# Kernel optimization log

Hardware: AMD Instinct MI355X
Metric: run time of the kernel (lower is better)

## Reference

```python
import jax, jax.numpy as jnp
import numpy as np

T, B, E, H = 2048, 2, 1024, 16
DH = E // H
SCALE = DH ** -0.5
NEG = jnp.finfo(jnp.float32).min


def setup_inputs() -> dict:
    key = jax.random.key(0)
    ks = jax.random.split(key, 10)
    s = 0.02
    query = jax.random.normal(ks[0], (T, B, E), dtype=jnp.float32)
    key_padding_mask = jax.random.randint(ks[1], (B, T), 0, 2).astype(bool)
    # causal additive mask, broadcastable over (bsz, heads, tgt, src)
    causal = jnp.triu(jnp.ones((T, T), dtype=bool), k=1)
    attn_mask = jnp.where(causal, NEG, 0.0).astype(jnp.float32)[None, None]
    Wq = jax.random.normal(ks[2], (E, E), jnp.float32) * s
    bq = jax.random.normal(ks[3], (E,), jnp.float32) * s
    Wk = jax.random.normal(ks[4], (E, E), jnp.float32) * s
    bk = jax.random.normal(ks[5], (E,), jnp.float32) * s
    Wv = jax.random.normal(ks[6], (E, E), jnp.float32) * s
    bv = jax.random.normal(ks[7], (E,), jnp.float32) * s
    Wo = jax.random.normal(ks[8], (E, E), jnp.float32) * s
    bo = jax.random.normal(ks[9], (E,), jnp.float32) * s
    return {"query": query, "key_padding_mask": key_padding_mask, "attn_mask": attn_mask,
            "Wq": Wq, "bq": bq, "Wk": Wk, "bk": bk, "Wv": Wv, "bv": bv, "Wo": Wo, "bo": bo}


def _heads(x):
    # [T, B, E] -> [B, H, T, DH]
    return x.reshape(T, B, H, DH).transpose(1, 2, 0, 3)


def reference(query, key_padding_mask, attn_mask, Wq, bq, Wk, bk, Wv, bv, Wo, bo):
    # projections (torch Linear: x @ W.T + b); q scaled as in module
    q = _heads((query @ Wq.T + bq) * SCALE)          # [B,H,T,DH]
    k = _heads(query @ Wk.T + bk)                    # [B,H,S,DH] (self-attn: S=T)
    v = _heads(query @ Wv.T + bv)
    scores = jnp.einsum('bhtd,bhsd->bhts', q, k)     # [B,H,T,S]
    scores = scores + attn_mask                      # additive causal mask
    # key_padding_mask True -> masked_fill with dtype min
    scores = jnp.where(key_padding_mask[:, None, None, :], NEG, scores)
    probs = jax.nn.softmax(scores, axis=-1)
    ctx = jnp.einsum('bhts,bhsd->bhtd', probs, v)    # [B,H,T,DH]
    ctx = ctx.transpose(2, 0, 1, 3).reshape(T, B, E) # back to [T,B,E]
    return ctx @ Wo.T + bo
```

## Files before the change

kernel.cpp:

```cpp
#include <hip/hip_runtime.h>
#include <hip/hip_bf16.h>
#include <stdint.h>

typedef unsigned short u16;
typedef uint32_t u32;
typedef unsigned long long u64;
typedef __attribute__((ext_vector_type(8))) short bf16x8;
typedef __attribute__((ext_vector_type(4))) float f32x4;
typedef __attribute__((ext_vector_type(16))) float f32x16;
typedef __attribute__((ext_vector_type(2))) unsigned int u32x2;
typedef __attribute__((ext_vector_type(4))) u32 u32x4;

#define T_SEQ 2048

__device__ __forceinline__ float bf2f(u16 u) {
  union { u32 i; float f; } v; v.i = ((u32)u) << 16; return v.f;
}
__device__ __forceinline__ u16 f2bf(float f) {
  union { float f; u32 i; } v; v.f = f;
  u32 u = v.i;
  return (u16)((u + 0x7fffu + ((u >> 16) & 1u)) >> 16);
}

#if __has_builtin(__builtin_amdgcn_exp2f)
#define EXP2F(x) __builtin_amdgcn_exp2f(x)
#else
#define EXP2F(x) exp2f(x)
#endif

__device__ __forceinline__ u32 permpack(float lo, float hi) {
#if __has_builtin(__builtin_amdgcn_perm)
  return __builtin_amdgcn_perm(__float_as_uint(hi), __float_as_uint(lo), 0x07060302u);
#else
  return (__float_as_uint(hi) & 0xFFFF0000u) | (__float_as_uint(lo) >> 16);
#endif
}

__device__ __forceinline__ void plswap(u32& a, u32& b) {
#if __has_builtin(__builtin_amdgcn_permlane32_swap)
  u32x2 r = __builtin_amdgcn_permlane32_swap(a, b, false, false);
  a = r[0]; b = r[1];
#else
  u32 ra = __shfl_xor(a, 32, 64), rb = __shfl_xor(b, 32, 64);
  const bool hi_ = (threadIdx.x & 32) != 0;
  u32 na = hi_ ? rb : a;
  u32 nb = hi_ ? b : ra;
  a = na; b = nb;
#endif
}
__device__ __forceinline__ float othhalf(float x, bool ishi) {
  u32 a = __float_as_uint(x), b = a;
  plswap(a, b);
  return __uint_as_float(ishi ? a : b);
}

__device__ __forceinline__ void gload_lds16(const void* g, void* l) {
  __builtin_amdgcn_global_load_lds(
      (const __attribute__((address_space(1))) void*)g,
      (__attribute__((address_space(3))) void*)l, 16, 0, 0);
}

__global__ __launch_bounds__(256) void cvt_kernel(const float* __restrict__ src,
                                                  u16* __restrict__ dst, int n) {
  int i = (blockIdx.x * 256 + threadIdx.x) * 4;
  if (i + 3 < n) {
    const float4 v = *(const float4*)(src + i);
    ushort4 o;
    o.x = f2bf(v.x); o.y = f2bf(v.y); o.z = f2bf(v.z); o.w = f2bf(v.w);
    *(ushort4*)(dst + i) = o;
  }
}

__global__ __launch_bounds__(256) void cvt4_kernel(
    const float* __restrict__ s0, const float* __restrict__ s1,
    const float* __restrict__ s2, const float* __restrict__ s3,
    u16* __restrict__ dst) {
  const int z = blockIdx.y;
  const float* src = (z == 0) ? s0 : (z == 1) ? s1 : (z == 2) ? s2 : s3;
  int i = (blockIdx.x * 256 + threadIdx.x) * 4;
  const float4 v = *(const float4*)(src + i);
  ushort4 o;
  o.x = f2bf(v.x); o.y = f2bf(v.y); o.z = f2bf(v.z); o.w = f2bf(v.w);
  *(ushort4*)(dst + (size_t)z * 1048576 + i) = o;
}

__device__ __forceinline__ void gemm_core_128x128(
    f32x4 acc[2][4], const u16* __restrict__ A, const u16* __restrict__ Bw,
    int bm, int bn, u16* As, u16* Bs)
{
  const int tid = threadIdx.x;
  const int w = tid >> 6, lane = tid & 63, g = lane >> 4, c = lane & 15;
  const int wr = (w & 3) * 32, wc = (w >> 2) * 64;

  auto stage = [&](int buf, int k0) {
    #pragma unroll
    for (int is = 0; is < 2; ++is) {
      int o = (is*8 + w)*1024 + lane*16;
      int row = o >> 7, c16 = (o >> 4) & 7;
      gload_lds16(A + (size_t)(bm*128 + row)*1024 + k0 + (c16 ^ (row & 7))*8,
                  (char*)As + buf*16384 + (is*8 + w)*1024);
    }
    #pragma unroll
    for (int is = 0; is < 2; ++is) {
      int o = (is*8 + w)*1024 + lane*16;
      int row = o >> 7, c16 = (o >> 4) & 7;
      gload_lds16(Bw + (size_t)(bn*128 + row)*1024 + k0 + (c16 ^ (row & 7))*8,
                  (char*)Bs + buf*16384 + (is*8 + w)*1024);
    }
  };

  stage(0, 0);
  asm volatile("s_waitcnt vmcnt(0)" ::: "memory");
  __syncthreads();

  for (int k0 = 0; k0 < 1024; k0 += 64) {
    const int cur = (k0 >> 6) & 1, nxt = cur ^ 1;
    const bool more = (k0 + 64 < 1024);
    if (more) stage(nxt, k0 + 64);

    bf16x8 af[2][2], bfr[4][2];
    #pragma unroll
    for (int mf = 0; mf < 2; ++mf)
      #pragma unroll
      for (int kc = 0; kc < 2; ++kc) {
        int row = wr + mf*16 + c;
        int colb = kc*64 + g*16;
        af[mf][kc] = *(const bf16x8*)((const char*)As + cur*16384 + row*128 + (colb ^ ((row & 7) << 4)));
      }
    #pragma unroll
    for (int nf = 0; nf < 4; ++nf)
      #pragma unroll
      for (int kc = 0; kc < 2; ++kc) {
        int row = wc + nf*16 + c;
        int colb = kc*64 + g*16;
        bfr[nf][kc] = *(const bf16x8*)((const char*)Bs + cur*16384 + row*128 + (colb ^ ((row & 7) << 4)));
      }
    #pragma unroll
    for (int mf = 0; mf < 2; ++mf)
      #pragma unroll
      for (int nf = 0; nf < 4; ++nf)
        #pragma unroll
        for (int kc = 0; kc < 2; ++kc)
          acc[mf][nf] = __builtin_amdgcn_mfma_f32_16x16x32_bf16(
              af[mf][kc], bfr[nf][kc], acc[mf][nf], 0, 0, 0);

    if (more) {
      asm volatile("s_waitcnt vmcnt(0)" ::: "memory");
      __syncthreads();
    }
  }
}

__global__ __launch_bounds__(512, 2) void gemm_qkv(
    const u16* __restrict__ Abf, const u16* __restrict__ Wbf,
    const float* __restrict__ bq, const float* __restrict__ bk,
    const float* __restrict__ bv, u16* __restrict__ qkvh)
{
  __shared__ __align__(16) u16 As[2][128*64];
  __shared__ __align__(16) u16 Bs[2][128*64];
  f32x4 acc[2][4];
  #pragma unroll
  for (int mf = 0; mf < 2; ++mf)
    #pragma unroll
    for (int nf = 0; nf < 4; ++nf) acc[mf][nf] = (f32x4){0.f,0.f,0.f,0.f};
  const int bx = blockIdx.x;
  const int bm = (bx & 7) * 4 + (bx >> 3);
  gemm_core_128x128(acc, Abf, Wbf, bm, blockIdx.y, &As[0][0], &Bs[0][0]);
  const int tid = threadIdx.x, w = tid >> 6, lane = tid & 63, g = lane >> 4, c = lane & 15;
  const int wr = (w & 3) * 32, wc = (w >> 2) * 64;
  #pragma unroll
  for (int mf = 0; mf < 2; ++mf)
    #pragma unroll
    for (int nf = 0; nf < 4; ++nf) {
      int col = blockIdx.y*128 + wc + nf*16 + c;
      int z = col >> 10, colz = col & 1023;
      const float* bias = (z == 0) ? bq : (z == 1) ? bk : bv;
      float bcol = bias[colz];
      float scl = (z == 0) ? 0.18033688011112043f : 1.0f;
      int h = colz >> 6, d = colz & 63;
      u16* dst = qkvh + (size_t)z * 4194304;
      #pragma unroll
      for (int r = 0; r < 4; ++r) {
        int row = bm*128 + wr + mf*16 + g*4 + r;
        int t = row >> 1, bb = row & 1;
        float v = (acc[mf][nf][r] + bcol) * scl;
        dst[(size_t)(bb*16 + h)*131072 + (size_t)t*64 + d] = f2bf(v);
      }
    }
}

__global__ __launch_bounds__(512, 2) void gemm_out(
    const u16* __restrict__ ctx2, const u16* __restrict__ Wobf,
    const float* __restrict__ bo, float* __restrict__ out)
{
  __shared__ __align__(16) u16 As[2][128*64];
  __shared__ __align__(16) u16 Bs[2][128*64];
  f32x4 acc[2][4];
  #pragma unroll
  for (int mf = 0; mf < 2; ++mf)
    #pragma unroll
    for (int nf = 0; nf < 4; ++nf) acc[mf][nf] = (f32x4){0.f,0.f,0.f,0.f};
  const int bx = blockIdx.x;
  const int bm = (bx & 7) * 4 + (bx >> 3);
  gemm_core_128x128(acc, ctx2, Wobf, bm, blockIdx.y, &As[0][0], &Bs[0][0]);
  const int tid = threadIdx.x, w = tid >> 6, lane = tid & 63, g = lane >> 4, c = lane & 15;
  const int wr = (w & 3) * 32, wc = (w >> 2) * 64;
  #pragma unroll
  for (int mf = 0; mf < 2; ++mf)
    #pragma unroll
    for (int nf = 0; nf < 4; ++nf) {
      int col = blockIdx.y*128 + wc + nf*16 + c;
      float bcol = bo[col];
      #pragma unroll
      for (int r = 0; r < 4; ++r) {
        int row = bm*128 + wr + mf*16 + g*4 + r;
        out[(size_t)row*1024 + col] = acc[mf][nf][r] + bcol;
      }
    }
}

__global__ __launch_bounds__(256) void vtrans_kernel(const u16* __restrict__ Vh,
                                                     u16* __restrict__ Vt,
                                                     float* __restrict__ vs) {
  __shared__ u16 tile[64][72];
  const int bh = blockIdx.x >> 5, tc = blockIdx.x & 31;
  const int t0 = tc * 64;
  const int tid = threadIdx.x;
  {
    const int tl = tid >> 2, d0 = (tid & 3) * 16;
    const u16* src = Vh + (size_t)bh*131072 + (size_t)(t0 + tl)*64 + d0;
    bf16x8 a = *(const bf16x8*)src;
    bf16x8 b2 = *(const bf16x8*)(src + 8);
    #pragma unroll
    for (int j = 0; j < 8; ++j) {
      tile[d0 + j][tl] = (u16)a[j];
      tile[d0 + 8 + j][tl] = (u16)b2[j];
    }
  }
  __syncthreads();
  {
    const int d = tid >> 2, tq = (tid & 3) * 16;
    bf16x8 o0, o1;
    float s = 0.f;
    #pragma unroll
    for (int j = 0; j < 8; ++j) {
      u16 x0 = tile[d][tq + j], x1 = tile[d][tq + 8 + j];
      o0[j] = (short)x0; o1[j] = (short)x1;
      s += bf2f(x0) + bf2f(x1);
    }
    u16* dst = Vt + (size_t)bh*131072 + (size_t)d*2048 + t0 + tq;
    *(bf16x8*)dst = o0;
    *(bf16x8*)(dst + 8) = o1;
    s += __shfl_xor(s, 1, 64);
    s += __shfl_xor(s, 2, 64);
    if ((tid & 3) == 0) atomicAdd(&vs[bh*64 + d], s);
  }
}

#define ZERO16 (f32x16){0.f,0.f,0.f,0.f,0.f,0.f,0.f,0.f,0.f,0.f,0.f,0.f,0.f,0.f,0.f,0.f}
#define NEGINF (-__builtin_inff())

__global__ __launch_bounds__(256, 2) void flash_attn(
    const u16* __restrict__ Qh, const u16* __restrict__ Kh,
    const u16* __restrict__ Vt, const int* __restrict__ kpm,
    const float* __restrict__ vsum, u16* __restrict__ ctx2,
    u16* __restrict__ pctx, float* __restrict__ pml)
{
  __shared__ __align__(16) u16 Kl[2][4096];
  __shared__ __align__(16) u16 Vl[2][4096];

  const int tid = threadIdx.x;
  const int w = tid >> 6, lane = tid & 63;
  const int l31 = lane & 31, hi = lane >> 5;

  const int id = blockIdx.x;
  const int xcd = id & 7, rest = id >> 3;
  const int bh = xcd * 4 + (rest & 3);
  const int pr = rest >> 2;
  const u64 k0t = 0x9AA5BBCC6DDEE7FFULL, k1t = 0x94883210ULL;
  const u64 m0t = 0x0102101021010210ULL, m1t = 0x12102222ULL;
  const int k  = (int)(((pr < 16) ? (k0t >> (pr*4)) : (k1t >> ((pr-16)*4))) & 15);
  const int md = (int)(((pr < 16) ? (m0t >> (pr*4)) : (m1t >> ((pr-16)*4))) & 3);
  const int NS = (md == 2) ? 1 : 2, ch = md & 1;

  const int ntmax = 2*k + 2;
  const int b = bh >> 4, h = bh & 15;
  const size_t hbase = (size_t)bh * 131072;
  int lo, hicap;
  if (NS == 1) { lo = 0; hicap = ntmax; }
  else { lo = ch ? (k+1) : 0; hicap = ch ? ntmax : (k+1); }
  const int q = 128*k + 32*w + l31;
  const int myNt = 2*k + 1 + (w >> 1);

  bf16x8 qfrag[4];
  #pragma unroll
  for (int kt = 0; kt < 4; ++kt)
    qfrag[kt] = *(const bf16x8*)(Qh + hbase + (size_t)q*64 + kt*16 + hi*8);

  {
    const int s0t = lo * 64;
    const int jb = (w & 1) * 4;
    if (w < 2) {
      #pragma unroll
      for (int is = 0; is < 4; ++is) {
        int o = (jb + is)*1024 + lane*16;
        int row = o >> 7, c16 = (o >> 4) & 7;
        gload_lds16(Kh + hbase + (size_t)(s0t + row)*64 + (c16 ^ (row & 7))*8,
                    (char*)Kl[0] + (jb + is)*1024);
      }
    } else {
      #pragma unroll
      for (int is = 0; is < 4; ++is) {
        int o = (jb + is)*1024 + lane*16;
        int row = o >> 7, c16 = (o >> 4) & 7;
        gload_lds16(Vt + hbase + (size_t)row*2048 + s0t + (c16 ^ (row & 7))*8,
                    (char*)Vl[0] + (jb + is)*1024);
      }
    }
  }
  int kpmv_cur = kpm[b*T_SEQ + lo*64 + lane];
  int kpmv_nxt = 0;
  __syncthreads();

  float mrow = NEGINF, lrow = 0.f;
  f32x16 cacc0 = ZERO16, cacc1 = ZERO16;

  for (int t = lo; t < hicap; ++t) {
    const int cur = (t - lo) & 1, nxt = cur ^ 1;
    const int s0 = t * 64;
    const bool notLast = (t + 1 < hicap);
    const bool diag = (t >= myNt - 1);

    if (notLast) {
      const int s0n = s0 + 64;
      const int jb = (w & 1) * 4;
      if (w < 2) {
        #pragma unroll
        for (int is = 0; is < 4; ++is) {
          int o = (jb + is)*1024 + lane*16;
          int row = o >> 7, c16 = (o >> 4) & 7;
          gload_lds16(Kh + hbase + (size_t)(s0n + row)*64 + (c16 ^ (row & 7))*8,
                      (char*)Kl[nxt] + (jb + is)*1024);
        }
      } else {
        #pragma unroll
        for (int is = 0; is < 4; ++is) {
          int o = (jb + is)*1024 + lane*16;
          int row = o >> 7, c16 = (o >> 4) & 7;
          gload_lds16(Vt + hbase + (size_t)row*2048 + s0n + (c16 ^ (row & 7))*8,
                      (char*)Vl[nxt] + (jb + is)*1024);
        }
      }
      kpmv_nxt = kpm[b*T_SEQ + s0n + lane];
    }

    u32 kill0 = 0, kill1 = 0;
    {
      const u64 mask = __ballot(kpmv_cur != 0);
      const u32 m0 = (u32)mask, m1 = (u32)(mask >> 32);
      const u64 m4 = mask >> 4;
      const u32 m4l = (u32)m4, m4h = (u32)(m4 >> 32);
      const u32 w0m = hi ? m4l : m0;
      const u32 w1m = hi ? m4h : m1;
      const int lim = q - s0 - 4*hi;
      #pragma unroll
      for (int m = 0; m < 4; ++m) {
        u32 nib0 = (w0m >> (m*8)) & 15u;
        u32 nib1 = (w1m >> (m*8)) & 15u;
        if (diag) {
          int t0c = lim - m*8;       int c0 = min(max(t0c + 1, 0), 4);
          int t1c = lim - 32 - m*8;  int c1 = min(max(t1c + 1, 0), 4);
          nib0 |= (0xFu << c0) & 0xFu;
          nib1 |= (0xFu << c1) & 0xFu;
        }
        kill0 |= nib0 << (m*4);
        kill1 |= nib1 << (m*4);
      }
    }
    f32x16 st0, st1;
    #pragma unroll
    for (int i = 0; i < 16; ++i) {
      st0[i] = ((kill0 >> i) & 1u) ? NEGINF : 0.f;
      st1[i] = ((kill1 >> i) & 1u) ? NEGINF : 0.f;
    }

    bf16x8 kreg[2][4], vf[2][4];
    #pragma unroll
    for (int sub = 0; sub < 2; ++sub)
      #pragma unroll
      for (int kt = 0; kt < 4; ++kt) {
        int row = sub*32 + l31;
        int colb = kt*32 + hi*16;
        kreg[sub][kt] = *(const bf16x8*)((const char*)Kl[cur] + row*128 + (colb ^ ((row & 7) << 4)));
        vf[sub][kt]   = *(const bf16x8*)((const char*)Vl[cur] + row*128 + (colb ^ ((row & 7) << 4)));
      }

    __builtin_amdgcn_s_setprio(1);
    #pragma unroll
    for (int kt = 0; kt < 4; ++kt) {
      st0 = __builtin_amdgcn_mfma_f32_32x32x16_bf16(kreg[0][kt], qfrag[kt], st0, 0, 0, 0);
      st1 = __builtin_amdgcn_mfma_f32_32x32x16_bf16(kreg[1][kt], qfrag[kt], st1, 0, 0, 0);
    }
    __builtin_amdgcn_s_setprio(0);

    {
      float t8[8];
      #pragma unroll
      for (int i = 0; i < 8; ++i)
        t8[i] = fmaxf(fmaxf(st0[i], st0[i+8]), fmaxf(st1[i], st1[i+8]));
      float t4a = fmaxf(t8[0], t8[4]), t4b = fmaxf(t8[1], t8[5]);
      float t4c = fmaxf(t8[2], t8[6]), t4d = fmaxf(t8[3], t8[7]);
      float rm = fmaxf(fmaxf(t4a, t4b), fmaxf(t4c, t4d));
      rm = fmaxf(rm, othhalf(rm, hi != 0));

      const bool need = (rm > mrow + 8.f) || (mrow < -1e30f);
      if (__any(need)) {
        const float mn = fmaxf(mrow, rm);
        const float sc = (mn < -1e30f) ? 1.f : EXP2F(mrow - mn);
        mrow = mn;
        lrow *= sc;
        #pragma unroll
        for (int i = 0; i < 16; ++i) { cacc0[i] *= sc; cacc1[i] *= sc; }
      }
      const bool dead = (mrow < -1e30f);
      float a0 = 0.f, a1 = 0.f, a2 = 0.f, a3 = 0.f;
      #pragma unroll
      for (int i = 0; i < 16; i += 4) {
        float p0 = dead ? 0.f : EXP2F(st0[i+0] - mrow); st0[i+0] = p0; a0 += p0;
        float p1 = dead ? 0.f : EXP2F(st0[i+1] - mrow); st0[i+1] = p1; a1 += p1;
        float p2 = dead ? 0.f : EXP2F(st0[i+2] - mrow); st0[i+2] = p2; a2 += p2;
        float p3 = dead ? 0.f : EXP2F(st0[i+3] - mrow); st0[i+3] = p3; a3 += p3;
      }
      #pragma unroll
      for (int i = 0; i < 16; i += 4) {
        float p0 = dead ? 0.f : EXP2F(st1[i+0] - mrow); st1[i+0] = p0; a0 += p0;
        float p1 = dead ? 0.f : EXP2F(st1[i+1] - mrow); st1[i+1] = p1; a1 += p1;
        float p2 = dead ? 0.f : EXP2F(st1[i+2] - mrow); st1[i+2] = p2; a2 += p2;
        float p3 = dead ? 0.f : EXP2F(st1[i+3] - mrow); st1[i+3] = p3; a3 += p3;
      }
      float ps = (a0 + a1) + (a2 + a3);
      ps += othhalf(ps, hi != 0);
      lrow += ps;
    }

    u32 pk[8][2];
    #pragma unroll
    for (int m = 0; m < 4; ++m) {
      pk[m][0]   = permpack(st0[m*4+0], st0[m*4+1]);
      pk[m][1]   = permpack(st0[m*4+2], st0[m*4+3]);
      pk[4+m][0] = permpack(st1[m*4+0], st1[m*4+1]);
      pk[4+m][1] = permpack(st1[m*4+2], st1[m*4+3]);
    }
    bf16x8 pf[4];
    #pragma unroll
    for (int ks = 0; ks < 4; ++ks) {
      u32 w0p = pk[2*ks][0], w2p = pk[2*ks+1][0];
      u32 w1p = pk[2*ks][1], w3p = pk[2*ks+1][1];
      plswap(w0p, w2p);
      plswap(w1p, w3p);
      u32x4 wv = {w0p, w1p, w2p, w3p};
      pf[ks] = __builtin_bit_cast(bf16x8, wv);
    }

    __builtin_amdgcn_s_setprio(1);
    #pragma unroll
    for (int ks = 0; ks < 4; ++ks)
      cacc0 = __builtin_amdgcn_mfma_f32_32x32x16_bf16(vf[0][ks], pf[ks], cacc0, 0, 0, 0);
    #pragma unroll
    for (int ks = 0; ks < 4; ++ks)
      cacc1 = __builtin_amdgcn_mfma_f32_32x32x16_bf16(vf[1][ks], pf[ks], cacc1, 0, 0, 0);
    __builtin_amdgcn_s_setprio(0);

    kpmv_cur = kpmv_nxt;
    if (notLast) __syncthreads();
  }

  if (NS == 1) {
    const bool dead = (lrow == 0.f);
    const float rl = dead ? 0.f : 1.f / lrow;
    #pragma unroll
    for (int subd = 0; subd < 2; ++subd) {
      #pragma unroll
      for (int m = 0; m < 4; ++m) {
        const int d0 = subd*32 + hi*4 + m*8;
        float v0 = (subd ? cacc1[m*4+0] : cacc0[m*4+0]) * rl;
        float v1 = (subd ? cacc1[m*4+1] : cacc0[m*4+1]) * rl;
        float v2 = (subd ? cacc1[m*4+2] : cacc0[m*4+2]) * rl;
        float v3 = (subd ? cacc1[m*4+3] : cacc0[m*4+3]) * rl;
        if (dead) {
          const float* vs = vsum + bh*64 + d0;
          v0 = vs[0] * (1.0f/2048.0f);
          v1 = vs[1] * (1.0f/2048.0f);
          v2 = vs[2] * (1.0f/2048.0f);
          v3 = vs[3] * (1.0f/2048.0f);
        }
        ushort4 o;
        o.x = f2bf(v0); o.y = f2bf(v1); o.z = f2bf(v2); o.w = f2bf(v3);
        *(ushort4*)(ctx2 + (size_t)(q*2 + b)*1024 + h*64 + d0) = o;
      }
    }
  } else {
    const int slot = ((bh << 3) + (k - 8))*2 + ch;
    const int row = w*32 + l31;
    u16* pc = pctx + ((size_t)slot*128 + row)*64;
    #pragma unroll
    for (int subd = 0; subd < 2; ++subd) {
      #pragma unroll
      for (int m = 0; m < 4; ++m) {
        const int d0 = subd*32 + hi*4 + m*8;
        const f32x16& cc = subd ? cacc1 : cacc0;
        ushort4 o;
        o.x = f2bf(cc[m*4+0]); o.y = f2bf(cc[m*4+1]);
        o.z = f2bf(cc[m*4+2]); o.w = f2bf(cc[m*4+3]);
        *(ushort4*)(pc + d0) = o;
      }
    }
    if (!hi) {
      float2 ml; ml.x = mrow; ml.y = lrow;
      *(float2*)(pml + ((size_t)slot*128 + row)*2) = ml;
    }
  }
}

__global__ __launch_bounds__(64) void combine_kernel(
    const u16* __restrict__ pctx, const float* __restrict__ pml,
    const float* __restrict__ vsum, u16* __restrict__ ctx2)
{
  const int qtm = blockIdx.x, bh = blockIdx.y;
  const int qt = 32 + qtm;
  const int k = qt >> 2, wq = qt & 3;
  const int b = bh >> 4, h = bh & 15;
  const int lane = threadIdx.x;
  const int qr = lane >> 1, d0 = (lane & 1) * 32;
  const int slot0 = ((bh << 3) + (k - 8))*2;
  const int row = wq*32 + qr;
  const float* ml0 = pml + ((size_t)slot0*128 + row)*2;
  const float* ml1 = pml + ((size_t)(slot0+1)*128 + row)*2;
  const float m1 = ml0[0], l1 = ml0[1];
  const float m2 = ml1[0], l2 = ml1[1];
  const float ms = fmaxf(m1, m2);
  bool dead = (ms == NEGINF);
  const float w1 = dead ? 0.f : EXP2F(m1 - ms);
  const float w2 = dead ? 0.f : EXP2F(m2 - ms);
  const float lt = w1*l1 + w2*l2;
  dead = dead || (lt == 0.f);
  const float rl = dead ? 0.f : 1.f / lt;
  const u16* c1 = pctx + ((size_t)slot0*128 + row)*64 + d0;
  const u16* c2 = pctx + ((size_t)(slot0+1)*128 + row)*64 + d0;
  const int qrow = qt*32 + qr;
  u16* dst = ctx2 + (size_t)(qrow*2 + b)*1024 + h*64 + d0;
  #pragma unroll
  for (int g2 = 0; g2 < 4; ++g2) {
    bf16x8 a = *(const bf16x8*)(c1 + g2*8);
    bf16x8 bb = *(const bf16x8*)(c2 + g2*8);
    bf16x8 o;
    #pragma unroll
    for (int j = 0; j < 8; ++j) {
      float v = (w1*bf2f((u16)a[j]) + w2*bf2f((u16)bb[j])) * rl;
      if (dead) v = vsum[bh*64 + d0 + g2*8 + j] * (1.0f/2048.0f);
      o[j] = (short)f2bf(v);
    }
    *(bf16x8*)(dst + g2*8) = o;
  }
}

extern "C" void kernel_launch(void* const* d_in, const int* in_sizes, int n_in,
                              void* d_out, int out_size, void* d_ws, size_t ws_size,
                              hipStream_t stream) {
  const float* query = (const float*)d_in[0];
  const int*   kpm   = (const int*)d_in[1];
  const float* Wq = (const float*)d_in[3];
  const float* bq = (const float*)d_in[4];
  const float* Wk = (const float*)d_in[5];
  const float* bk = (const float*)d_in[6];
  const float* Wv = (const float*)d_in[7];
  const float* bv = (const float*)d_in[8];
  const float* Wo = (const float*)d_in[9];
  const float* bo = (const float*)d_in[10];

  char* ws = (char*)d_ws;
  u16*   qbf  = (u16*)(ws);
  u16*   Vt   = (u16*)(ws);
  u16*   wbf  = (u16*)(ws + 8388608);
  u16*   qkvh = (u16*)(ws + 16777216);
  u16*   pctx = (u16*)(ws + 33554432);
  u16*   ctx2 = (u16*)(ws + 41943040);
  float* vsum = (float*)(ws + 50331648);
  float* pml  = (float*)(ws + 50339840);

  cvt_kernel<<<dim3(4096), 256, 0, stream>>>(query, qbf, 4194304);
  cvt4_kernel<<<dim3(1024, 4), 256, 0, stream>>>(Wq, Wk, Wv, Wo, wbf);

  hipMemsetAsync(vsum, 0, 2048 * sizeof(float), stream);

  gemm_qkv<<<dim3(32, 24), 512, 0, stream>>>(qbf, wbf, bq, bk, bv, qkvh);
  vtrans_kernel<<<dim3(1024), 256, 0, stream>>>(qkvh + 2*4194304, Vt, vsum);
  flash_attn<<<dim3(768), 256, 0, stream>>>(qkvh, qkvh + 1*4194304,
                                            Vt, kpm, vsum, ctx2, pctx, pml);
  combine_kernel<<<dim3(32, 32), 64, 0, stream>>>(pctx, pml, vsum, ctx2);
  gemm_out<<<dim3(32, 8), 512, 0, stream>>>(ctx2, wbf + 3*1048576, bo, (float*)d_out);
}
```

Measured before the change: 137.4 us.

## Rebalance attention split-KV into up to 4 chunks, fuse conversions, single-buffer GEMM

Flash attention now takes its query-tile and chunk assignments from a lookup table. Longer causal rows are split into up to four KV chunks, so the launch grows from 768 to 1280 blocks and per-block work is more even. Chunk 0 writes straight into ctx2 and the other chunks write partials into reused workspace. The combine kernel now merges up to four partials per row. The two fp32-to-bf16 conversion launches are fused into one. The GEMM core drops LDS double buffering in favour of a simpler load-sync-compute loop, which cuts LDS use but exposes global-load latency.

Result: slower. 141.8 us (+3.2%).

```diff
diff --git a/kernel.cpp b/kernel.cpp
--- a/kernel.cpp
+++ b/kernel.cpp
@@ -60,28 +60,25 @@
       (__attribute__((address_space(3))) void*)l, 16, 0, 0);
 }
 
-__global__ __launch_bounds__(256) void cvt_kernel(const float* __restrict__ src,
-                                                  u16* __restrict__ dst, int n) {
-  int i = (blockIdx.x * 256 + threadIdx.x) * 4;
-  if (i + 3 < n) {
-    const float4 v = *(const float4*)(src + i);
-    ushort4 o;
-    o.x = f2bf(v.x); o.y = f2bf(v.y); o.z = f2bf(v.z); o.w = f2bf(v.w);
-    *(ushort4*)(dst + i) = o;
-  }
-}
-
-__global__ __launch_bounds__(256) void cvt4_kernel(
-    const float* __restrict__ s0, const float* __restrict__ s1,
-    const float* __restrict__ s2, const float* __restrict__ s3,
-    u16* __restrict__ dst) {
-  const int z = blockIdx.y;
-  const float* src = (z == 0) ? s0 : (z == 1) ? s1 : (z == 2) ? s2 : s3;
-  int i = (blockIdx.x * 256 + threadIdx.x) * 4;
+__global__ __launch_bounds__(256) void cvt5_kernel(
+    const float* __restrict__ qsrc, const float* __restrict__ w0,
+    const float* __restrict__ w1, const float* __restrict__ w2,
+    const float* __restrict__ w3, u16* __restrict__ qbf, u16* __restrict__ wbf) {
+  const int bx = blockIdx.x;
+  const float* src; u16* dst; int i;
+  if (bx < 4096) {
+    src = qsrc; dst = qbf; i = (bx*256 + threadIdx.x)*4;
+  } else {
+    int t = bx - 4096;
+    int z = t >> 10;
+    src = (z == 0) ? w0 : (z == 1) ? w1 : (z == 2) ? w2 : w3;
+    dst = wbf + (size_t)z * 1048576;
+    i = ((t & 1023)*256 + threadIdx.x)*4;
+  }
   const float4 v = *(const float4*)(src + i);
   ushort4 o;
   o.x = f2bf(v.x); o.y = f2bf(v.y); o.z = f2bf(v.z); o.w = f2bf(v.w);
-  *(ushort4*)(dst + (size_t)z * 1048576 + i) = o;
+  *(ushort4*)(dst + i) = o;
 }
 
 __device__ __forceinline__ void gemm_core_128x128(
@@ -91,33 +88,23 @@
   const int tid = threadIdx.x;
   const int w = tid >> 6, lane = tid & 63, g = lane >> 4, c = lane & 15;
   const int wr = (w & 3) * 32, wc = (w >> 2) * 64;
-
-  auto stage = [&](int buf, int k0) {
+  for (int k0 = 0; k0 < 1024; k0 += 64) {
+    __syncthreads();
     #pragma unroll
     for (int is = 0; is < 2; ++is) {
       int o = (is*8 + w)*1024 + lane*16;
       int row = o >> 7, c16 = (o >> 4) & 7;
       gload_lds16(A + (size_t)(bm*128 + row)*1024 + k0 + (c16 ^ (row & 7))*8,
-                  (char*)As + buf*16384 + (is*8 + w)*1024);
+                  (char*)As + (is*8 + w)*1024);
     }
     #pragma unroll
     for (int is = 0; is < 2; ++is) {
       int o = (is*8 + w)*1024 + lane*16;
       int row = o >> 7, c16 = (o >> 4) & 7;
       gload_lds16(Bw + (size_t)(bn*128 + row)*1024 + k0 + (c16 ^ (row & 7))*8,
-                  (char*)Bs + buf*16384 + (is*8 + w)*1024);
-    }
-  };
-
-  stage(0, 0);
-  asm volatile("s_waitcnt vmcnt(0)" ::: "memory");
-  __syncthreads();
-
-  for (int k0 = 0; k0 < 1024; k0 += 64) {
-    const int cur = (k0 >> 6) & 1, nxt = cur ^ 1;
-    const bool more = (k0 + 64 < 1024);
-    if (more) stage(nxt, k0 + 64);
-
+                  (char*)Bs + (is*8 + w)*1024);
+    }
+    __syncthreads();
     bf16x8 af[2][2], bfr[4][2];
     #pragma unroll
     for (int mf = 0; mf < 2; ++mf)
@@ -125,7 +112,7 @@
       for (int kc = 0; kc < 2; ++kc) {
         int row = wr + mf*16 + c;
         int colb = kc*64 + g*16;
-        af[mf][kc] = *(const bf16x8*)((const char*)As + cur*16384 + row*128 + (colb ^ ((row & 7) << 4)));
+        af[mf][kc] = *(const bf16x8*)((const char*)As + row*128 + (colb ^ ((row & 7) << 4)));
       }
     #pragma unroll
     for (int nf = 0; nf < 4; ++nf)
@@ -133,7 +120,7 @@
       for (int kc = 0; kc < 2; ++kc) {
         int row = wc + nf*16 + c;
         int colb = kc*64 + g*16;
-        bfr[nf][kc] = *(const bf16x8*)((const char*)Bs + cur*16384 + row*128 + (colb ^ ((row & 7) << 4)));
+        bfr[nf][kc] = *(const bf16x8*)((const char*)Bs + row*128 + (colb ^ ((row & 7) << 4)));
       }
     #pragma unroll
     for (int mf = 0; mf < 2; ++mf)
@@ -143,11 +130,6 @@
         for (int kc = 0; kc < 2; ++kc)
           acc[mf][nf] = __builtin_amdgcn_mfma_f32_16x16x32_bf16(
               af[mf][kc], bfr[nf][kc], acc[mf][nf], 0, 0, 0);
-
-    if (more) {
-      asm volatile("s_waitcnt vmcnt(0)" ::: "memory");
-      __syncthreads();
-    }
   }
 }
 
@@ -156,8 +138,8 @@
     const float* __restrict__ bq, const float* __restrict__ bk,
     const float* __restrict__ bv, u16* __restrict__ qkvh)
 {
-  __shared__ __align__(16) u16 As[2][128*64];
-  __shared__ __align__(16) u16 Bs[2][128*64];
+  __shared__ __align__(16) u16 As[128*64];
+  __shared__ __align__(16) u16 Bs[128*64];
   f32x4 acc[2][4];
   #pragma unroll
   for (int mf = 0; mf < 2; ++mf)
@@ -165,7 +147,7 @@
     for (int nf = 0; nf < 4; ++nf) acc[mf][nf] = (f32x4){0.f,0.f,0.f,0.f};
   const int bx = blockIdx.x;
   const int bm = (bx & 7) * 4 + (bx >> 3);
-  gemm_core_128x128(acc, Abf, Wbf, bm, blockIdx.y, &As[0][0], &Bs[0][0]);
+  gemm_core_128x128(acc, Abf, Wbf, bm, blockIdx.y, As, Bs);
   const int tid = threadIdx.x, w = tid >> 6, lane = tid & 63, g = lane >> 4, c = lane & 15;
   const int wr = (w & 3) * 32, wc = (w >> 2) * 64;
   #pragma unroll
@@ -193,8 +175,8 @@
     const u16* __restrict__ ctx2, const u16* __restrict__ Wobf,
     const float* __restrict__ bo, float* __restrict__ out)
 {
-  __shared__ __align__(16) u16 As[2][128*64];
-  __shared__ __align__(16) u16 Bs[2][128*64];
+  __shared__ __align__(16) u16 As[128*64];
+  __shared__ __align__(16) u16 Bs[128*64];
   f32x4 acc[2][4];
   #pragma unroll
   for (int mf = 0; mf < 2; ++mf)
@@ -202,7 +184,7 @@
     for (int nf = 0; nf < 4; ++nf) acc[mf][nf] = (f32x4){0.f,0.f,0.f,0.f};
   const int bx = blockIdx.x;
   const int bm = (bx & 7) * 4 + (bx >> 3);
-  gemm_core_128x128(acc, ctx2, Wobf, bm, blockIdx.y, &As[0][0], &Bs[0][0]);
+  gemm_core_128x128(acc, ctx2, Wobf, bm, blockIdx.y, As, Bs);
   const int tid = threadIdx.x, w = tid >> 6, lane = tid & 63, g = lane >> 4, c = lane & 15;
   const int wr = (w & 3) * 32, wc = (w >> 2) * 64;
   #pragma unroll
@@ -260,11 +242,30 @@
 #define ZERO16 (f32x16){0.f,0.f,0.f,0.f,0.f,0.f,0.f,0.f,0.f,0.f,0.f,0.f,0.f,0.f,0.f,0.f}
 #define NEGINF (-__builtin_inff())
 
+__device__ const unsigned char CTBL[40] = {
+  60, 44, 28, 12, 57, 59, 52, 37,
+  61, 45, 29, 42, 40, 56, 53, 38,
+  62, 46, 24, 25, 41, 58, 54, 49,
+  63,  8, 20, 21, 32, 34, 55, 51,
+   0,  4, 16, 17, 33, 36, 48, 50 };
+
+__device__ __forceinline__ int pctx_off(int k, int ch) {
+  if (k < 8)  return (k - 4);
+  if (k < 12) return 4 + (k - 8)*2 + (ch - 1);
+  return 12 + (k - 12)*3 + (ch - 1);
+}
+__device__ __forceinline__ int pml_off(int k, int ch) {
+  if (k < 8)  return (k - 4)*2 + ch;
+  if (k < 12) return 8 + (k - 8)*3 + ch;
+  return 20 + (k - 12)*4 + ch;
+}
+
 __global__ __launch_bounds__(256, 2) void flash_attn(
     const u16* __restrict__ Qh, const u16* __restrict__ Kh,
     const u16* __restrict__ Vt, const int* __restrict__ kpm,
     const float* __restrict__ vsum, u16* __restrict__ ctx2,
-    u16* __restrict__ pctx, float* __restrict__ pml)
+    u16* __restrict__ pctxA, u16* __restrict__ pctxB,
+    float* __restrict__ pml)
 {
   __shared__ __align__(16) u16 Kl[2][4096];
   __shared__ __align__(16) u16 Vl[2][4096];
@@ -276,19 +277,15 @@
   const int id = blockIdx.x;
   const int xcd = id & 7, rest = id >> 3;
   const int bh = xcd * 4 + (rest & 3);
-  const int pr = rest >> 2;
-  const u64 k0t = 0x9AA5BBCC6DDEE7FFULL, k1t = 0x94883210ULL;
-  const u64 m0t = 0x0102101021010210ULL, m1t = 0x12102222ULL;
-  const int k  = (int)(((pr < 16) ? (k0t >> (pr*4)) : (k1t >> ((pr-16)*4))) & 15);
-  const int md = (int)(((pr < 16) ? (m0t >> (pr*4)) : (m1t >> ((pr-16)*4))) & 3);
-  const int NS = (md == 2) ? 1 : 2, ch = md & 1;
-
-  const int ntmax = 2*k + 2;
+  const int cidx = rest >> 2;
+  const int v_tbl = CTBL[cidx];
+  const int k = v_tbl >> 2, ch = v_tbl & 3;
+  const int NS = (k >> 2) + 1;
+  const int nt = 2*k + 2;
+  const int lo = (nt * ch) / NS, hicap = (nt * (ch + 1)) / NS;
+
   const int b = bh >> 4, h = bh & 15;
   const size_t hbase = (size_t)bh * 131072;
-  int lo, hicap;
-  if (NS == 1) { lo = 0; hicap = ntmax; }
-  else { lo = ch ? (k+1) : 0; hicap = ch ? ntmax : (k+1); }
   const int q = 128*k + 32*w + l31;
   const int myNt = 2*k + 1 + (w >> 1);
 
@@ -500,9 +497,20 @@
       }
     }
   } else {
-    const int slot = ((bh << 3) + (k - 8))*2 + ch;
     const int row = w*32 + l31;
-    u16* pc = pctx + ((size_t)slot*128 + row)*64;
+    if (!hi) {
+      float2 ml; ml.x = mrow; ml.y = lrow;
+      *(float2*)(pml + (size_t)(bh*36 + pml_off(k, ch))*256 + row*2) = ml;
+    }
+    u16* pc;
+    if (ch == 0) {
+      pc = ctx2 + (size_t)(q*2 + b)*1024 + h*64;
+    } else {
+      const int slot = bh*24 + pctx_off(k, ch);
+      pc = (slot < 512) ? (pctxA + (size_t)slot*8192)
+                        : (pctxB + (size_t)(slot - 512)*8192);
+      pc += (size_t)row*64;
+    }
     #pragma unroll
     for (int subd = 0; subd < 2; ++subd) {
       #pragma unroll
@@ -515,49 +523,67 @@
         *(ushort4*)(pc + d0) = o;
       }
     }
-    if (!hi) {
-      float2 ml; ml.x = mrow; ml.y = lrow;
-      *(float2*)(pml + ((size_t)slot*128 + row)*2) = ml;
-    }
-  }
-}
-
-__global__ __launch_bounds__(64) void combine_kernel(
-    const u16* __restrict__ pctx, const float* __restrict__ pml,
-    const float* __restrict__ vsum, u16* __restrict__ ctx2)
+  }
+}
+
+__global__ __launch_bounds__(256) void combine_kernel(
+    const u16* __restrict__ pctxA, const u16* __restrict__ pctxB,
+    const float* __restrict__ pml, const float* __restrict__ vsum,
+    u16* __restrict__ ctx2)
 {
-  const int qtm = blockIdx.x, bh = blockIdx.y;
-  const int qt = 32 + qtm;
-  const int k = qt >> 2, wq = qt & 3;
+  const int k = 4 + blockIdx.x;
+  const int bh = blockIdx.y;
+  const int NS = (k >> 2) + 1;
   const int b = bh >> 4, h = bh & 15;
-  const int lane = threadIdx.x;
-  const int qr = lane >> 1, d0 = (lane & 1) * 32;
-  const int slot0 = ((bh << 3) + (k - 8))*2;
-  const int row = wq*32 + qr;
-  const float* ml0 = pml + ((size_t)slot0*128 + row)*2;
-  const float* ml1 = pml + ((size_t)(slot0+1)*128 + row)*2;
-  const float m1 = ml0[0], l1 = ml0[1];
-  const float m2 = ml1[0], l2 = ml1[1];
-  const float ms = fmaxf(m1, m2);
-  bool dead = (ms == NEGINF);
-  const float w1 = dead ? 0.f : EXP2F(m1 - ms);
-  const float w2 = dead ? 0.f : EXP2F(m2 - ms);
-  const float lt = w1*l1 + w2*l2;
+  const int tid = threadIdx.x;
+  const int row = tid >> 1, dh = (tid & 1) * 32;
+  const int q = k*128 + row;
+
+  const float* mlb = pml + (size_t)(bh*36 + pml_off(k, 0))*256 + row*2;
+  float m0v = mlb[0],        l0v = mlb[1];
+  float m1v = mlb[256+0],    l1v = mlb[256+1];
+  float m2v = NEGINF, l2v = 0.f, m3v = NEGINF, l3v = 0.f;
+  if (NS > 2) { m2v = mlb[512+0];  l2v = mlb[512+1]; }
+  if (NS > 3) { m3v = mlb[768+0];  l3v = mlb[768+1]; }
+  float ms = fmaxf(fmaxf(m0v, m1v), fmaxf(m2v, m3v));
+  bool dead = (ms < -1e30f);
+  const float w0 = dead ? 0.f : EXP2F(m0v - ms);
+  const float w1 = dead ? 0.f : EXP2F(m1v - ms);
+  const float w2 = (dead || NS <= 2) ? 0.f : EXP2F(m2v - ms);
+  const float w3 = (dead || NS <= 3) ? 0.f : EXP2F(m3v - ms);
+  const float lt = w0*l0v + w1*l1v + w2*l2v + w3*l3v;
   dead = dead || (lt == 0.f);
   const float rl = dead ? 0.f : 1.f / lt;
-  const u16* c1 = pctx + ((size_t)slot0*128 + row)*64 + d0;
-  const u16* c2 = pctx + ((size_t)(slot0+1)*128 + row)*64 + d0;
-  const int qrow = qt*32 + qr;
-  u16* dst = ctx2 + (size_t)(qrow*2 + b)*1024 + h*64 + d0;
+
+  u16* dst = ctx2 + (size_t)(q*2 + b)*1024 + h*64 + dh;
+  const u16* pc1; const u16* pc2 = nullptr; const u16* pc3 = nullptr;
+  {
+    const int s1 = bh*24 + pctx_off(k, 1);
+    pc1 = ((s1 < 512) ? (pctxA + (size_t)s1*8192) : (pctxB + (size_t)(s1-512)*8192))
+          + (size_t)row*64 + dh;
+    if (NS > 2) {
+      const int s2 = bh*24 + pctx_off(k, 2);
+      pc2 = ((s2 < 512) ? (pctxA + (size_t)s2*8192) : (pctxB + (size_t)(s2-512)*8192))
+            + (size_t)row*64 + dh;
+    }
+    if (NS > 3) {
+      const int s3 = bh*24 + pctx_off(k, 3);
+      pc3 = ((s3 < 512) ? (pctxA + (size_t)s3*8192) : (pctxB + (size_t)(s3-512)*8192))
+            + (size_t)row*64 + dh;
+    }
+  }
   #pragma unroll
   for (int g2 = 0; g2 < 4; ++g2) {
-    bf16x8 a = *(const bf16x8*)(c1 + g2*8);
-    bf16x8 bb = *(const bf16x8*)(c2 + g2*8);
+    bf16x8 a0 = *(const bf16x8*)(dst + g2*8);
+    bf16x8 a1 = *(const bf16x8*)(pc1 + g2*8);
     bf16x8 o;
     #pragma unroll
     for (int j = 0; j < 8; ++j) {
-      float v = (w1*bf2f((u16)a[j]) + w2*bf2f((u16)bb[j])) * rl;
-      if (dead) v = vsum[bh*64 + d0 + g2*8 + j] * (1.0f/2048.0f);
+      float v = w0*bf2f((u16)a0[j]) + w1*bf2f((u16)a1[j]);
+      if (NS > 2) v += w2*bf2f((u16)((const u16*)pc2)[g2*8 + j]);
+      if (NS > 3) v += w3*bf2f((u16)((const u16*)pc3)[g2*8 + j]);
+      v *= rl;
+      if (dead) v = vsum[bh*64 + dh + g2*8 + j] * (1.0f/2048.0f);
       o[j] = (short)f2bf(v);
     }
     *(bf16x8*)(dst + g2*8) = o;
@@ -579,24 +605,24 @@
   const float* bo = (const float*)d_in[10];
 
   char* ws = (char*)d_ws;
-  u16*   qbf  = (u16*)(ws);
-  u16*   Vt   = (u16*)(ws);
-  u16*   wbf  = (u16*)(ws + 8388608);
-  u16*   qkvh = (u16*)(ws + 16777216);
-  u16*   pctx = (u16*)(ws + 33554432);
-  u16*   ctx2 = (u16*)(ws + 41943040);
-  float* vsum = (float*)(ws + 50331648);
-  float* pml  = (float*)(ws + 50339840);
-
-  cvt_kernel<<<dim3(4096), 256, 0, stream>>>(query, qbf, 4194304);
-  cvt4_kernel<<<dim3(1024, 4), 256, 0, stream>>>(Wq, Wk, Wv, Wo, wbf);
+  u16*   qbf   = (u16*)(ws);
+  u16*   Vt    = (u16*)(ws);
+  u16*   wbf   = (u16*)(ws + 8388608);
+  u16*   pctxB = (u16*)(ws + 8388608);
+  u16*   qkvh  = (u16*)(ws + 16777216);
+  u16*   pctxA = (u16*)(ws + 33554432);
+  u16*   ctx2  = (u16*)(ws + 41943040);
+  float* vsum  = (float*)(ws + 50331648);
+  float* pml   = (float*)(ws + 50339840);
+
+  cvt5_kernel<<<dim3(8192), 256, 0, stream>>>(query, Wq, Wk, Wv, Wo, qbf, wbf);
 
   hipMemsetAsync(vsum, 0, 2048 * sizeof(float), stream);
 
   gemm_qkv<<<dim3(32, 24), 512, 0, stream>>>(qbf, wbf, bq, bk, bv, qkvh);
   vtrans_kernel<<<dim3(1024), 256, 0, stream>>>(qkvh + 2*4194304, Vt, vsum);
-  flash_attn<<<dim3(768), 256, 0, stream>>>(qkvh, qkvh + 1*4194304,
-                                            Vt, kpm, vsum, ctx2, pctx, pml);
-  combine_kernel<<<dim3(32, 32), 64, 0, stream>>>(pctx, pml, vsum, ctx2);
+  flash_attn<<<dim3(1280), 256, 0, stream>>>(qkvh, qkvh + 1*4194304,
+                                             Vt, kpm, vsum, ctx2, pctxA, pctxB, pml);
+  combine_kernel<<<dim3(12, 32), 256, 0, stream>>>(pctxA, pctxB, pml, vsum, ctx2);
   gemm_out<<<dim3(32, 8), 512, 0, stream>>>(ctx2, wbf + 3*1048576, bo, (float*)d_out);
 }
```
